# Kernel tuning notes

Measured on AMD Instinct MI355X. Metric: run time of the kernel, lower is better.

The kernel has to match this reference:

```python
import jax, jax.numpy as jnp
import numpy as np

B, N, D = 2, 2048, 1024   # batch, seq, input_dim
H, DK, DV = 8, 128, 1024  # heads, qk_dim, v_dim (v_dim == input_dim for residual)


def setup_inputs() -> dict:
    key = jax.random.key(0)
    kx, kq, kk, kv = jax.random.split(key, 4)
    scale = 0.02
    x = jax.random.normal(kx, (B, N, D), dtype=jnp.float32)
    # torch nn.Linear weights are [out_features, in_features]; stacked over heads.
    Wq = jax.random.normal(kq, (H, DK, D), dtype=jnp.float32) * scale
    Wk = jax.random.normal(kk, (H, DK, D), dtype=jnp.float32) * scale
    Wv = jax.random.normal(kv, (H, DV, D), dtype=jnp.float32) * scale
    return {"x": x, "Wq": Wq, "Wk": Wk, "Wv": Wv}


def reference(x, Wq, Wk, Wv):
    # x: [B, N, D]; Wq/Wk: [H, DK, D]; Wv: [H, DV, D]
    n = x.shape[-2]
    Q = jnp.einsum('bnd,hed->bhne', x, Wq)  # [B,H,N,DK]
    K = jnp.einsum('bnd,hed->bhne', x, Wk)  # [B,H,N,DK]
    V = jnp.einsum('bnd,hvd->bhnv', x, Wv)  # [B,H,N,DV]
    scores = jnp.einsum('bhne,bhme->bhnm', Q, K)  # [B,H,N,N]
    # causal mask: masked entries set to mask_value=0.0, then relu, then /N
    causal = jnp.tril(jnp.ones((n, n), dtype=bool))
    sim = jnp.where(causal, jax.nn.relu(scores), jnp.float32(0.0)) / jnp.float32(n)
    # sum of per-head outputs added to residual
    head_out = jnp.einsum('bhnm,bhmv->bnv', sim, V)  # [B,N,DV]
    return x + head_out
```

## Files before the change

### kernel.cpp

```cpp
#include <hip/hip_runtime.h>

typedef __attribute__((ext_vector_type(8))) short bf16x8;
typedef __attribute__((ext_vector_type(4))) float floatx4;

__device__ __forceinline__ unsigned short f2bf(float f) {
  unsigned int u = __builtin_bit_cast(unsigned int, f);
  unsigned int r = (u + 0x7fffu + ((u >> 16) & 1u)) >> 16;
  return (unsigned short)r;
}

__device__ __forceinline__ unsigned int pack2(float a, float b) {
  return (unsigned int)f2bf(a) | ((unsigned int)f2bf(b) << 16);
}

__device__ __forceinline__ void gload16(const void* g, void* l) {
  __builtin_amdgcn_global_load_lds(
      (__attribute__((address_space(1))) void*)g,
      (__attribute__((address_space(3))) void*)l, 16, 0, 0);
}

__device__ __forceinline__ void barrier_v0_lgkm() {
  asm volatile("s_waitcnt vmcnt(0) lgkmcnt(0)" ::: "memory");
  __builtin_amdgcn_s_barrier();
  __builtin_amdgcn_sched_barrier(0);
}

__global__ __launch_bounds__(256) void convert_all(
    const float4* __restrict__ x4,
    const float4* __restrict__ wq4, const float4* __restrict__ wk4,
    const float4* __restrict__ wv4,
    uint2* __restrict__ xb4, uint2* __restrict__ wqkb4, uint2* __restrict__ wvb4,
    float4* __restrict__ out4)
{
  const int NX = 2 * 2048 * 1024 / 4;
  const int NQK = 8 * 256 * 1024 / 4;
  const int NV = 8 * 1024 * 1024 / 4;
  const int total = NX + NQK + NV;
  const float inv_n = 1.0f / 2048.0f;
  for (int i = blockIdx.x * 256 + threadIdx.x; i < total; i += gridDim.x * 256) {
    float4 f; uint2* dst;
    if (i < NX) {
      f = x4[i]; dst = &xb4[i];
      out4[i] = f;
    } else if (i < NX + NQK) {
      int j = i - NX;
      int c = j & 255;
      int row = j >> 8;
      int h = row >> 8, r = row & 255;
      f = (r < 128) ? wq4[(h * 128 + r) * 256 + c] : wk4[(h * 128 + r - 128) * 256 + c];
      dst = &wqkb4[j];
    } else {
      int j = i - NX - NQK;
      f = wv4[j];
      f.x *= inv_n; f.y *= inv_n; f.z *= inv_n; f.w *= inv_n;
      dst = &wvb4[j];
    }
    uint2 p; p.x = pack2(f.x, f.y); p.y = pack2(f.z, f.w);
    *dst = p;
  }
}

__global__ __launch_bounds__(256) void init_out(const float4* __restrict__ x,
                                                float4* __restrict__ out, int n4) {
  for (int i = blockIdx.x * 256 + threadIdx.x; i < n4; i += gridDim.x * 256)
    out[i] = x[i];
}

__global__ __launch_bounds__(512, 2) void gemm8(
    const unsigned short* __restrict__ xb,
    const unsigned short* __restrict__ Wqkb,
    const unsigned short* __restrict__ Wvb,
    unsigned short* __restrict__ Qb, unsigned short* __restrict__ Kb,
    unsigned short* __restrict__ Vtb)
{
  __shared__ __align__(16) unsigned short LA[2][2][128 * 64];
  __shared__ __align__(16) unsigned short LB[2][2][128 * 64];
  const int bid = blockIdx.x;
  const int t = threadIdx.x;
  const int l = t & 63, w = t >> 6;
  const int l16 = l & 15, lq = l >> 4;
  const int wm = w & 1, wn = w >> 1;

  const unsigned short *Ag, *Bg;
  unsigned short *C0, *C1; long ld0, ld1; int split;
  if (bid < 128) {
    int z = bid & 15, br = bid >> 4;
    int b = z >> 3, h = z & 7;
    Ag = xb + (long)b * 2048 * 1024 + (long)br * 256 * 1024;
    Bg = Wqkb + (long)h * 256 * 1024;
    C0 = Qb + (long)z * 2048 * 128 + (long)br * 256 * 128;
    C1 = Kb + (long)z * 2048 * 128 + (long)br * 256 * 128;
    ld0 = 128; ld1 = 128; split = 128;
  } else {
    int v = bid - 128;
    int z = v & 15, rc = v >> 4;
    int bx = rc & 3, by = rc >> 2;
    int b = z >> 3, h = z & 7;
    Ag = Wvb + (long)h * 1024 * 1024 + (long)bx * 256 * 1024;
    Bg = xb + (long)b * 2048 * 1024 + (long)by * 256 * 1024;
    C0 = Vtb + (long)z * 1024 * 2048 + (long)bx * 256 * 2048 + by * 256;
    C1 = C0; ld0 = 2048; ld1 = 2048; split = 1 << 30;
  }

  int rr[2], kk[2], cb[2];
#pragma unroll
  for (int i = 0; i < 2; i++) {
    int c = i * 512 + t;
    rr[i] = c >> 3;
    int k8 = c & 7;
    kk[i] = (k8 ^ (((rr[i] >> 2) & 3) << 1)) * 8;
    cb[i] = (i * 512 + w * 64) * 8;
  }
  auto STAGE = [&](const unsigned short* OP, unsigned short* dstbuf, int kt, int half) {
#pragma unroll
    for (int i = 0; i < 2; i++)
      gload16(OP + (long)(half * 128 + rr[i]) * 1024 + kt * 64 + kk[i],
              dstbuf + cb[i]);
  };
  auto RD = [&](const unsigned short* buf, int fr, int ks) -> bf16x8 {
    int r = fr * 16 + l16;
    int k8 = ks * 4 + lq;
    int k8s = k8 ^ (((r >> 2) & 3) << 1);
    return *reinterpret_cast<const bf16x8*>(buf + r * 64 + k8s * 8);
  };

  floatx4 acc[8][4] = {};
  const int bfr = (wn & 1) * 4;

  STAGE(Ag, LA[0][0], 0, 0); STAGE(Ag, LA[0][1], 0, 1);
  STAGE(Bg, LB[0][0], 0, 0); STAGE(Bg, LB[0][1], 0, 1);
  asm volatile("s_waitcnt vmcnt(0)" ::: "memory");
  __builtin_amdgcn_s_barrier();
  __builtin_amdgcn_sched_barrier(0);

  for (int kt = 0; kt < 16; kt++) {
    const int d = kt & 1, nd = d ^ 1;
    const unsigned short* myA = LA[d][wm];
    const unsigned short* myB = LB[d][wn >> 1];
    const bool more = (kt + 1 < 16);
    bf16x8 a0[4][2], a1[4][2], b0[2][2], b1[2][2];

#pragma unroll
    for (int fr = 0; fr < 4; fr++)
#pragma unroll
      for (int ks = 0; ks < 2; ks++) a0[fr][ks] = RD(myA, fr, ks);
#pragma unroll
    for (int fc = 0; fc < 2; fc++)
#pragma unroll
      for (int ks = 0; ks < 2; ks++) b0[fc][ks] = RD(myB, bfr + fc, ks);
    if (more) { STAGE(Ag, LA[nd][0], kt + 1, 0); STAGE(Ag, LA[nd][1], kt + 1, 1); }
    __builtin_amdgcn_s_barrier();
    asm volatile("s_waitcnt lgkmcnt(0)" ::: "memory");
    __builtin_amdgcn_sched_barrier(0);
    __builtin_amdgcn_s_setprio(1);
#pragma unroll
    for (int fr = 0; fr < 4; fr++)
#pragma unroll
      for (int fc = 0; fc < 2; fc++)
#pragma unroll
        for (int ks = 0; ks < 2; ks++)
          acc[fr][fc] = __builtin_amdgcn_mfma_f32_16x16x32_bf16(
              a0[fr][ks], b0[fc][ks], acc[fr][fc], 0, 0, 0);
    __builtin_amdgcn_s_setprio(0);
    __builtin_amdgcn_s_barrier();

#pragma unroll
    for (int fc = 0; fc < 2; fc++)
#pragma unroll
      for (int ks = 0; ks < 2; ks++) b1[fc][ks] = RD(myB, bfr + 2 + fc, ks);
    if (more) { STAGE(Bg, LB[nd][0], kt + 1, 0); STAGE(Bg, LB[nd][1], kt + 1, 1); }
    __builtin_amdgcn_s_barrier();
    asm volatile("s_waitcnt lgkmcnt(0)" ::: "memory");
    __builtin_amdgcn_sched_barrier(0);
    __builtin_amdgcn_s_setprio(1);
#pragma unroll
    for (int fr = 0; fr < 4; fr++)
#pragma unroll
      for (int fc = 0; fc < 2; fc++)
#pragma unroll
        for (int ks = 0; ks < 2; ks++)
          acc[fr][2 + fc] = __builtin_amdgcn_mfma_f32_16x16x32_bf16(
              a0[fr][ks], b1[fc][ks], acc[fr][2 + fc], 0, 0, 0);
    __builtin_amdgcn_s_setprio(0);
    __builtin_amdgcn_s_barrier();

#pragma unroll
    for (int fr = 0; fr < 4; fr++)
#pragma unroll
      for (int ks = 0; ks < 2; ks++) a1[fr][ks] = RD(myA, 4 + fr, ks);
    __builtin_amdgcn_s_barrier();
    asm volatile("s_waitcnt lgkmcnt(0)" ::: "memory");
    __builtin_amdgcn_sched_barrier(0);
    __builtin_amdgcn_s_setprio(1);
#pragma unroll
    for (int fr = 0; fr < 4; fr++)
#pragma unroll
      for (int fc = 0; fc < 2; fc++)
#pragma unroll
        for (int ks = 0; ks < 2; ks++)
          acc[4 + fr][fc] = __builtin_amdgcn_mfma_f32_16x16x32_bf16(
              a1[fr][ks], b0[fc][ks], acc[4 + fr][fc], 0, 0, 0);
    __builtin_amdgcn_s_setprio(0);
    __builtin_amdgcn_s_barrier();

    __builtin_amdgcn_s_setprio(1);
#pragma unroll
    for (int fr = 0; fr < 4; fr++)
#pragma unroll
      for (int fc = 0; fc < 2; fc++)
#pragma unroll
        for (int ks = 0; ks < 2; ks++)
          acc[4 + fr][2 + fc] = __builtin_amdgcn_mfma_f32_16x16x32_bf16(
              a1[fr][ks], b1[fc][ks], acc[4 + fr][2 + fc], 0, 0, 0);
    __builtin_amdgcn_s_setprio(0);
    asm volatile("s_waitcnt vmcnt(0)" ::: "memory");
    __builtin_amdgcn_s_barrier();
    __builtin_amdgcn_sched_barrier(0);
  }

#pragma unroll
  for (int fr = 0; fr < 8; fr++)
#pragma unroll
    for (int fc = 0; fc < 4; fc++)
#pragma unroll
      for (int j = 0; j < 4; j++) {
        int row = wm * 128 + fr * 16 + lq * 4 + j;
        int col = wn * 64 + fc * 16 + l16;
        unsigned short v = f2bf(acc[fr][fc][j]);
        if (col < split) C0[(long)row * ld0 + col] = v;
        else             C1[(long)row * ld1 + (col - split)] = v;
      }
}

__global__ __launch_bounds__(256) void gemm_bt(
    const float* __restrict__ Abase, long sAb, long sAh,
    const float* __restrict__ Bbase, long sBb, long sBh,
    unsigned short* __restrict__ Cbase, long sC,
    int M, int Nc, int K, int H, float cscale)
{
  int z = blockIdx.z;
  int b = z / H, h = z % H;
  const float* A  = Abase + (long)b * sAb + (long)h * sAh;
  const float* Bm = Bbase + (long)b * sBb + (long)h * sBh;
  unsigned short* C = Cbase + (long)z * sC;
  int tRow = blockIdx.x * 128;
  int tCol = blockIdx.y * 128;
  __shared__ __align__(16) unsigned short LA[128 * 72];
  __shared__ __align__(16) unsigned short LB[128 * 72];
  int t = threadIdx.x;
  int l = t & 63, w = t >> 6;
  int wr = w >> 1, wc = w & 1;
  int l16 = l & 15, lq = l >> 4;
  floatx4 acc[4][4] = {};
  for (int k0 = 0; k0 < K; k0 += 64) {
    __syncthreads();
    for (int i = 0; i < 8; i++) {
      int lin = i * 256 + t;
      int row = lin >> 4;
      int c4  = lin & 15;
      float4 va = *reinterpret_cast<const float4*>(A + (long)(tRow + row) * K + k0 + c4 * 4);
      uint2 pa; pa.x = pack2(va.x, va.y); pa.y = pack2(va.z, va.w);
      *reinterpret_cast<uint2*>(&LA[row * 72 + c4 * 4]) = pa;
      float4 vb = *reinterpret_cast<const float4*>(Bm + (long)(tCol + row) * K + k0 + c4 * 4);
      uint2 pb; pb.x = pack2(vb.x, vb.y); pb.y = pack2(vb.z, vb.w);
      *reinterpret_cast<uint2*>(&LB[row * 72 + c4 * 4]) = pb;
    }
    __syncthreads();
    for (int kk = 0; kk < 2; kk++) {
      bf16x8 af[4], bfr[4];
      for (int m = 0; m < 4; m++)
        af[m]  = *reinterpret_cast<const bf16x8*>(&LA[(wr * 64 + m * 16 + l16) * 72 + kk * 32 + lq * 8]);
      for (int n = 0; n < 4; n++)
        bfr[n] = *reinterpret_cast<const bf16x8*>(&LB[(wc * 64 + n * 16 + l16) * 72 + kk * 32 + lq * 8]);
      for (int m = 0; m < 4; m++)
        for (int n = 0; n < 4; n++)
          acc[m][n] = __builtin_amdgcn_mfma_f32_16x16x32_bf16(af[m], bfr[n], acc[m][n], 0, 0, 0);
    }
  }
  for (int m = 0; m < 4; m++)
    for (int n = 0; n < 4; n++)
      for (int j = 0; j < 4; j++) {
        int row = tRow + wr * 64 + m * 16 + lq * 4 + j;
        int col = tCol + wc * 64 + n * 16 + l16;
        C[(long)row * Nc + col] = f2bf(acc[m][n][j] * cscale);
      }
}

__global__ __launch_bounds__(256) void gemm_qk(
    const float* __restrict__ x,
    const float* __restrict__ Wq, const float* __restrict__ Wk,
    unsigned short* __restrict__ Qb, unsigned short* __restrict__ Kb)
{
  int z = blockIdx.z;
  int b = z >> 3, h = z & 7;
  const float* A  = x + (long)b * 2048 * 1024;
  const float* Bm = (blockIdx.y ? Wk : Wq) + (long)h * 128 * 1024;
  unsigned short* C = (blockIdx.y ? Kb : Qb) + (long)z * 2048 * 128;
  int tRow = blockIdx.x * 128;
  __shared__ __align__(16) unsigned short LA[128 * 72];
  __shared__ __align__(16) unsigned short LB[128 * 72];
  int t = threadIdx.x;
  int l = t & 63, w = t >> 6;
  int wr = w >> 1, wc = w & 1;
  int l16 = l & 15, lq = l >> 4;
  floatx4 acc[4][4] = {};
  const int K = 1024;
  for (int k0 = 0; k0 < K; k0 += 64) {
    __syncthreads();
    for (int i = 0; i < 8; i++) {
      int lin = i * 256 + t;
      int row = lin >> 4;
      int c4  = lin & 15;
      float4 va = *reinterpret_cast<const float4*>(A + (long)(tRow + row) * K + k0 + c4 * 4);
      uint2 pa; pa.x = pack2(va.x, va.y); pa.y = pack2(va.z, va.w);
      *reinterpret_cast<uint2*>(&LA[row * 72 + c4 * 4]) = pa;
      float4 vb = *reinterpret_cast<const float4*>(Bm + (long)row * K + k0 + c4 * 4);
      uint2 pb; pb.x = pack2(vb.x, vb.y); pb.y = pack2(vb.z, vb.w);
      *reinterpret_cast<uint2*>(&LB[row * 72 + c4 * 4]) = pb;
    }
    __syncthreads();
    for (int kk = 0; kk < 2; kk++) {
      bf16x8 af[4], bfr[4];
      for (int m = 0; m < 4; m++)
        af[m]  = *reinterpret_cast<const bf16x8*>(&LA[(wr * 64 + m * 16 + l16) * 72 + kk * 32 + lq * 8]);
      for (int n = 0; n < 4; n++)
        bfr[n] = *reinterpret_cast<const bf16x8*>(&LB[(wc * 64 + n * 16 + l16) * 72 + kk * 32 + lq * 8]);
      for (int m = 0; m < 4; m++)
        for (int n = 0; n < 4; n++)
          acc[m][n] = __builtin_amdgcn_mfma_f32_16x16x32_bf16(af[m], bfr[n], acc[m][n], 0, 0, 0);
    }
  }
  for (int m = 0; m < 4; m++)
    for (int n = 0; n < 4; n++)
      for (int j = 0; j < 4; j++) {
        int row = tRow + wr * 64 + m * 16 + lq * 4 + j;
        int col = wc * 64 + n * 16 + l16;
        C[(long)row * 128 + col] = f2bf(acc[m][n][j]);
      }
}

__global__ __launch_bounds__(256, 2) void attn_fused(
    const unsigned short* __restrict__ Qb,
    const unsigned short* __restrict__ Kb,
    const unsigned short* __restrict__ Vtb,
    float* __restrict__ out)
{
  const int bid = blockIdx.x;
  const int z = bid & 15;
  const int pair = (bid >> 4) & 15;
  const int vb = bid >> 8;
  const int b = z >> 3;
  const int t = threadIdx.x;
  const int l = t & 63, w = t >> 6;
  const int l16 = l & 15, lq = l >> 4;
  const int wm = w & 1, wn = w >> 1;
  const int swz = l16 & 7;

  __shared__ __align__(16) unsigned short LK[2][64 * 128];
  __shared__ __align__(16) unsigned short LV[256 * 64];
  __shared__ __align__(16) unsigned short LP[64 * 64];

  const unsigned short* Qz = Qb + (long)z * 2048 * 128;
  const unsigned short* Kh = Kb + (long)z * 2048 * 128;
  const unsigned short* Vh = Vtb + (long)z * 1024 * 2048 + (long)(vb * 256) * 2048;

  int ksrc[4], kdst[4];
#pragma unroll
  for (int i = 0; i < 4; i++) {
    int chunk = i * 256 + w * 64 + l;
    int r = chunk >> 4, c = chunk & 15;
    int cs = ((c & 7) ^ (r & 7)) | (c & 8);
    ksrc[i] = r * 128 + cs * 8;
    kdst[i] = (i * 256 + w * 64) * 8;
  }
  int vsrc[8], vdst[8];
#pragma unroll
  for (int i = 0; i < 8; i++) {
    int chunk = i * 256 + w * 64 + l;
    int r = chunk >> 3, c = chunk & 7;
    int cs = c ^ (r & 7);
    vsrc[i] = r * 2048 + cs * 8;
    vdst[i] = (i * 256 + w * 64) * 8;
  }

  int cur = 0;
  for (int hf = 0; hf < 2; hf++) {
    const int T = hf ? (31 - pair) : pair;
    const unsigned short* Qh = Qz + (long)T * 64 * 128;
    bf16x8 aQ[2][4];
#pragma unroll
    for (int sn = 0; sn < 2; sn++)
#pragma unroll
      for (int ke = 0; ke < 4; ke++)
        aQ[sn][ke] = *reinterpret_cast<const bf16x8*>(
            Qh + (long)(wn * 32 + sn * 16 + l16) * 128 + ke * 32 + lq * 8);
    floatx4 acc[4][4] = {};
#pragma unroll
    for (int i = 0; i < 4; i++)
      gload16(Kh + ksrc[i], &LK[cur][kdst[i]]);
    for (int M = 0; M <= T; M++) {
      barrier_v0_lgkm();
#pragma unroll
      for (int i = 0; i < 8; i++)
        gload16(Vh + M * 64 + vsrc[i], &LV[vdst[i]]);
      if (M < T) {
#pragma unroll
        for (int i = 0; i < 4; i++)
          gload16(Kh + (M + 1) * 8192 + ksrc[i], &LK[cur ^ 1][kdst[i]]);
      }
      const unsigned short* LKc = LK[cur];
      floatx4 sacc[2][2] = {{{}, {}}, {{}, {}}};
      __builtin_amdgcn_s_setprio(1);
#pragma unroll
      for (int ke = 0; ke < 4; ke++) {
        bf16x8 kf[2];
#pragma unroll
        for (int sm = 0; sm < 2; sm++) {
          int chunk = 4 * ke + lq;
          kf[sm] = *reinterpret_cast<const bf16x8*>(
              &LKc[(wm * 32 + sm * 16 + l16) * 128 +
                   ((((chunk & 7) ^ swz) | (chunk & 8)) * 8)]);
        }
#pragma unroll
        for (int sm = 0; sm < 2; sm++)
#pragma unroll
          for (int sn = 0; sn < 2; sn++)
            sacc[sm][sn] = __builtin_amdgcn_mfma_f32_16x16x32_bf16(
                kf[sm], aQ[sn][ke], sacc[sm][sn], 0, 0, 0);
      }
      __builtin_amdgcn_s_setprio(0);
      const bool diag = (M == T);
#pragma unroll
      for (int sm = 0; sm < 2; sm++)
#pragma unroll
        for (int sn = 0; sn < 2; sn++) {
          floatx4 v = sacc[sm][sn];
          float f0 = fmaxf(v[0], 0.0f), f1 = fmaxf(v[1], 0.0f);
          float f2 = fmaxf(v[2], 0.0f), f3 = fmaxf(v[3], 0.0f);
          if (diag) {
            int mm = wm * 32 + sm * 16 + lq * 4;
            int nn = wn * 32 + sn * 16 + l16;
            if (mm + 0 > nn) f0 = 0.0f;
            if (mm + 1 > nn) f1 = 0.0f;
            if (mm + 2 > nn) f2 = 0.0f;
            if (mm + 3 > nn) f3 = 0.0f;
          }
          unsigned int p0, p1;
          asm("v_cvt_pk_bf16_f32 %0, %1, %2" : "=v"(p0) : "v"(f0), "v"(f1));
          asm("v_cvt_pk_bf16_f32 %0, %1, %2" : "=v"(p1) : "v"(f2), "v"(f3));
          uint2 pk; pk.x = p0; pk.y = p1;
          int row = wn * 32 + sn * 16 + l16;
          int cs = wm * 32 + sm * 16 + lq * 4;
          *reinterpret_cast<uint2*>(
              &LP[row * 64 + (((cs >> 3) ^ (row & 7)) * 8) + (cs & 7)]) = pk;
        }
      if (M < T) {
        asm volatile("s_waitcnt vmcnt(4) lgkmcnt(0)" ::: "memory");
      } else {
        asm volatile("s_waitcnt vmcnt(0) lgkmcnt(0)" ::: "memory");
      }
      __builtin_amdgcn_s_barrier();
      __builtin_amdgcn_sched_barrier(0);
      __builtin_amdgcn_s_setprio(1);
#pragma unroll
      for (int km = 0; km < 2; km++) {
        bf16x8 aP[4], bV[4];
#pragma unroll
        for (int nf = 0; nf < 4; nf++)
          aP[nf] = *reinterpret_cast<const bf16x8*>(
              &LP[(nf * 16 + l16) * 64 + (((4 * km + lq) ^ swz) * 8)]);
#pragma unroll
        for (int vf = 0; vf < 4; vf++)
          bV[vf] = *reinterpret_cast<const bf16x8*>(
              &LV[(w * 64 + vf * 16 + l16) * 64 + (((4 * km + lq) ^ swz) * 8)]);
#pragma unroll
        for (int nf = 0; nf < 4; nf++)
#pragma unroll
          for (int vf = 0; vf < 4; vf++)
            acc[nf][vf] = __builtin_amdgcn_mfma_f32_16x16x32_bf16(
                aP[nf], bV[vf], acc[nf][vf], 0, 0, 0);
      }
      __builtin_amdgcn_s_setprio(0);
      cur ^= 1;
    }
#pragma unroll
    for (int nf = 0; nf < 4; nf++)
#pragma unroll
      for (int vf = 0; vf < 4; vf++)
#pragma unroll
        for (int j = 0; j < 4; j++) {
          int n = T * 64 + nf * 16 + lq * 4 + j;
          int v = vb * 256 + w * 64 + vf * 16 + l16;
          long idx = ((long)b * 2048 + n) * 1024 + v;
          unsafeAtomicAdd(&out[idx], acc[nf][vf][j]);
        }
  }
}

extern "C" void kernel_launch(void* const* d_in, const int* in_sizes, int n_in,
                              void* d_out, int out_size, void* d_ws, size_t ws_size,
                              hipStream_t stream) {
  const float* x  = (const float*)d_in[0];
  const float* Wq = (const float*)d_in[1];
  const float* Wk = (const float*)d_in[2];
  const float* Wv = (const float*)d_in[3];
  float* out = (float*)d_out;
  const size_t MB = 1u << 20;
  dim3 blk(256);

  if (ws_size >= 104 * MB) {
    unsigned short* Vtb  = (unsigned short*)d_ws;
    unsigned short* Wqkb = (unsigned short*)d_ws;
    unsigned short* Qb   = (unsigned short*)((char*)d_ws + 64 * MB);
    unsigned short* Kb   = (unsigned short*)((char*)d_ws + 72 * MB);
    unsigned short* xb   = (unsigned short*)((char*)d_ws + 80 * MB);
    unsigned short* Wvb  = (unsigned short*)((char*)d_ws + 88 * MB);

    convert_all<<<dim3(2048), blk, 0, stream>>>(
        (const float4*)x, (const float4*)Wq, (const float4*)Wk, (const float4*)Wv,
        (uint2*)xb, (uint2*)Wqkb, (uint2*)Wvb, (float4*)out);
    gemm8<<<dim3(640), dim3(512), 0, stream>>>(xb, Wqkb, Wvb, Qb, Kb, Vtb);
    attn_fused<<<dim3(1024), blk, 0, stream>>>(Qb, Kb, Vtb, out);
  } else {
    unsigned short* Qb  = (unsigned short*)d_ws;
    unsigned short* Kb  = Qb + (size_t)2 * 8 * 2048 * 128;
    unsigned short* Vtb = Kb + (size_t)2 * 8 * 2048 * 128;
    init_out<<<dim3(1024), blk, 0, stream>>>(
        (const float4*)x, (float4*)out, 2 * 2048 * 1024 / 4);
    gemm_qk<<<dim3(16, 2, 16), blk, 0, stream>>>(x, Wq, Wk, Qb, Kb);
    gemm_bt<<<dim3(8, 16, 16), blk, 0, stream>>>(
        Wv, 0, (long)1024 * 1024, x, (long)2048 * 1024, 0,
        Vtb, (long)1024 * 2048, 1024, 2048, 1024, 8, 1.0f / 2048.0f);
    attn_fused<<<dim3(1024), blk, 0, stream>>>(Qb, Kb, Vtb, out);
  }
}
```

Baseline: 277.5 us.

## Double attention query tile to 128 rows to halve K/V reloads

The fused attention kernel now processes 128 query rows per block instead of 64, with each wave covering 64 query columns. Every K and V tile loaded into shared memory is reused across twice as many queries, which halves K/V global traffic and the number of atomic-add passes over the output. The grid shrinks from 1024 to 512 blocks. The costs are higher accumulator register pressure (8x4 fragments), a larger shared P buffer, and extra masked work on the two diagonal tiles, all of which may reduce occupancy.

```diff
diff --git a/kernel.cpp b/kernel.cpp
--- a/kernel.cpp
+++ b/kernel.cpp
@@ -347,8 +347,8 @@
 {
   const int bid = blockIdx.x;
   const int z = bid & 15;
-  const int pair = (bid >> 4) & 15;
-  const int vb = bid >> 8;
+  const int qp = (bid >> 4) & 7;
+  const int vb = bid >> 7;
   const int b = z >> 3;
   const int t = threadIdx.x;
   const int l = t & 63, w = t >> 6;
@@ -358,7 +358,7 @@
 
   __shared__ __align__(16) unsigned short LK[2][64 * 128];
   __shared__ __align__(16) unsigned short LV[256 * 64];
-  __shared__ __align__(16) unsigned short LP[64 * 64];
+  __shared__ __align__(16) unsigned short LP[128 * 64];
 
   const unsigned short* Qz = Qb + (long)z * 2048 * 128;
   const unsigned short* Kh = Kb + (long)z * 2048 * 128;
@@ -385,31 +385,32 @@
 
   int cur = 0;
   for (int hf = 0; hf < 2; hf++) {
-    const int T = hf ? (31 - pair) : pair;
-    const unsigned short* Qh = Qz + (long)T * 64 * 128;
-    bf16x8 aQ[2][4];
-#pragma unroll
-    for (int sn = 0; sn < 2; sn++)
+    const int qb = hf ? (15 - qp) : qp;
+    const int MT = 2 * qb + 1;
+    const unsigned short* Qh = Qz + (long)qb * 128 * 128;
+    bf16x8 aQ[4][4];
+#pragma unroll
+    for (int sn = 0; sn < 4; sn++)
 #pragma unroll
       for (int ke = 0; ke < 4; ke++)
         aQ[sn][ke] = *reinterpret_cast<const bf16x8*>(
-            Qh + (long)(wn * 32 + sn * 16 + l16) * 128 + ke * 32 + lq * 8);
-    floatx4 acc[4][4] = {};
+            Qh + (long)(wn * 64 + sn * 16 + l16) * 128 + ke * 32 + lq * 8);
+    floatx4 acc[8][4] = {};
 #pragma unroll
     for (int i = 0; i < 4; i++)
       gload16(Kh + ksrc[i], &LK[cur][kdst[i]]);
-    for (int M = 0; M <= T; M++) {
+    for (int M = 0; M <= MT; M++) {
       barrier_v0_lgkm();
 #pragma unroll
       for (int i = 0; i < 8; i++)
         gload16(Vh + M * 64 + vsrc[i], &LV[vdst[i]]);
-      if (M < T) {
+      if (M < MT) {
 #pragma unroll
         for (int i = 0; i < 4; i++)
           gload16(Kh + (M + 1) * 8192 + ksrc[i], &LK[cur ^ 1][kdst[i]]);
       }
       const unsigned short* LKc = LK[cur];
-      floatx4 sacc[2][2] = {{{}, {}}, {{}, {}}};
+      floatx4 sacc[2][4] = {};
       __builtin_amdgcn_s_setprio(1);
 #pragma unroll
       for (int ke = 0; ke < 4; ke++) {
@@ -424,22 +425,23 @@
 #pragma unroll
         for (int sm = 0; sm < 2; sm++)
 #pragma unroll
-          for (int sn = 0; sn < 2; sn++)
+          for (int sn = 0; sn < 4; sn++)
             sacc[sm][sn] = __builtin_amdgcn_mfma_f32_16x16x32_bf16(
                 kf[sm], aQ[sn][ke], sacc[sm][sn], 0, 0, 0);
       }
       __builtin_amdgcn_s_setprio(0);
-      const bool diag = (M == T);
+      const bool diag = (M >= 2 * qb);
+      const int mbase = (M - 2 * qb) * 64;
 #pragma unroll
       for (int sm = 0; sm < 2; sm++)
 #pragma unroll
-        for (int sn = 0; sn < 2; sn++) {
+        for (int sn = 0; sn < 4; sn++) {
           floatx4 v = sacc[sm][sn];
           float f0 = fmaxf(v[0], 0.0f), f1 = fmaxf(v[1], 0.0f);
           float f2 = fmaxf(v[2], 0.0f), f3 = fmaxf(v[3], 0.0f);
           if (diag) {
-            int mm = wm * 32 + sm * 16 + lq * 4;
-            int nn = wn * 32 + sn * 16 + l16;
+            int mm = mbase + wm * 32 + sm * 16 + lq * 4;
+            int nn = wn * 64 + sn * 16 + l16;
             if (mm + 0 > nn) f0 = 0.0f;
             if (mm + 1 > nn) f1 = 0.0f;
             if (mm + 2 > nn) f2 = 0.0f;
@@ -449,12 +451,12 @@
           asm("v_cvt_pk_bf16_f32 %0, %1, %2" : "=v"(p0) : "v"(f0), "v"(f1));
           asm("v_cvt_pk_bf16_f32 %0, %1, %2" : "=v"(p1) : "v"(f2), "v"(f3));
           uint2 pk; pk.x = p0; pk.y = p1;
-          int row = wn * 32 + sn * 16 + l16;
+          int row = wn * 64 + sn * 16 + l16;
           int cs = wm * 32 + sm * 16 + lq * 4;
           *reinterpret_cast<uint2*>(
               &LP[row * 64 + (((cs >> 3) ^ (row & 7)) * 8) + (cs & 7)]) = pk;
         }
-      if (M < T) {
+      if (M < MT) {
         asm volatile("s_waitcnt vmcnt(4) lgkmcnt(0)" ::: "memory");
       } else {
         asm volatile("s_waitcnt vmcnt(0) lgkmcnt(0)" ::: "memory");
@@ -464,32 +466,32 @@
       __builtin_amdgcn_s_setprio(1);
 #pragma unroll
       for (int km = 0; km < 2; km++) {
-        bf16x8 aP[4], bV[4];
-#pragma unroll
-        for (int nf = 0; nf < 4; nf++)
-          aP[nf] = *reinterpret_cast<const bf16x8*>(
-              &LP[(nf * 16 + l16) * 64 + (((4 * km + lq) ^ swz) * 8)]);
+        bf16x8 bV[4];
 #pragma unroll
         for (int vf = 0; vf < 4; vf++)
           bV[vf] = *reinterpret_cast<const bf16x8*>(
               &LV[(w * 64 + vf * 16 + l16) * 64 + (((4 * km + lq) ^ swz) * 8)]);
 #pragma unroll
-        for (int nf = 0; nf < 4; nf++)
+        for (int nf = 0; nf < 8; nf++) {
+          int row = nf * 16 + l16;
+          bf16x8 aP = *reinterpret_cast<const bf16x8*>(
+              &LP[row * 64 + (((4 * km + lq) ^ (row & 7)) * 8)]);
 #pragma unroll
           for (int vf = 0; vf < 4; vf++)
             acc[nf][vf] = __builtin_amdgcn_mfma_f32_16x16x32_bf16(
-                aP[nf], bV[vf], acc[nf][vf], 0, 0, 0);
+                aP, bV[vf], acc[nf][vf], 0, 0, 0);
+        }
       }
       __builtin_amdgcn_s_setprio(0);
       cur ^= 1;
     }
 #pragma unroll
-    for (int nf = 0; nf < 4; nf++)
+    for (int nf = 0; nf < 8; nf++)
 #pragma unroll
       for (int vf = 0; vf < 4; vf++)
 #pragma unroll
         for (int j = 0; j < 4; j++) {
-          int n = T * 64 + nf * 16 + lq * 4 + j;
+          int n = qb * 128 + nf * 16 + lq * 4 + j;
           int v = vb * 256 + w * 64 + vf * 16 + l16;
           long idx = ((long)b * 2048 + n) * 1024 + v;
           unsafeAtomicAdd(&out[idx], acc[nf][vf][j]);
@@ -520,7 +522,7 @@
         (const float4*)x, (const float4*)Wq, (const float4*)Wk, (const float4*)Wv,
         (uint2*)xb, (uint2*)Wqkb, (uint2*)Wvb, (float4*)out);
     gemm8<<<dim3(640), dim3(512), 0, stream>>>(xb, Wqkb, Wvb, Qb, Kb, Vtb);
-    attn_fused<<<dim3(1024), blk, 0, stream>>>(Qb, Kb, Vtb, out);
+    attn_fused<<<dim3(512), blk, 0, stream>>>(Qb, Kb, Vtb, out);
   } else {
     unsigned short* Qb  = (unsigned short*)d_ws;
     unsigned short* Kb  = Qb + (size_t)2 * 8 * 2048 * 128;
@@ -531,6 +533,6 @@
     gemm_bt<<<dim3(8, 16, 16), blk, 0, stream>>>(
         Wv, 0, (long)1024 * 1024, x, (long)2048 * 1024, 0,
         Vtb, (long)1024 * 2048, 1024, 2048, 1024, 8, 1.0f / 2048.0f);
-    attn_fused<<<dim3(1024), blk, 0, stream>>>(Qb, Kb, Vtb, out);
-  }
-}
+    attn_fused<<<dim3(512), blk, 0, stream>>>(Qb, Kb, Vtb, out);
+  }
+}
```

New measurement: 425.5 us. +53.3%, slower.

## Widen attention key tile to 128 with 512-thread blocks

Applied to the files above, without the earlier changes.

The fused attention kernel now uses 8 waves per block and processes 128 keys per iteration instead of 64. This halves the number of loop iterations, barriers and pipeline steps per query tile. Each wave now owns 32 value columns instead of 64, and the score computation is split across 4 key-row groups. The cost is larger LDS buffers, about 144KB per block, so only one block fits per CU. The final 128-key chunk of even-indexed query tiles is half wasted on fully masked work.

```diff
diff --git a/kernel.cpp b/kernel.cpp
--- a/kernel.cpp
+++ b/kernel.cpp
@@ -339,7 +339,7 @@
       }
 }
 
-__global__ __launch_bounds__(256, 2) void attn_fused(
+__global__ __launch_bounds__(512) void attn_fused(
     const unsigned short* __restrict__ Qb,
     const unsigned short* __restrict__ Kb,
     const unsigned short* __restrict__ Vtb,
@@ -353,12 +353,11 @@
   const int t = threadIdx.x;
   const int l = t & 63, w = t >> 6;
   const int l16 = l & 15, lq = l >> 4;
-  const int wm = w & 1, wn = w >> 1;
-  const int swz = l16 & 7;
-
-  __shared__ __align__(16) unsigned short LK[2][64 * 128];
-  __shared__ __align__(16) unsigned short LV[256 * 64];
-  __shared__ __align__(16) unsigned short LP[64 * 64];
+  const int wm = w & 3, wn = w >> 2;
+
+  __shared__ __align__(16) unsigned short LK[2][128 * 128];
+  __shared__ __align__(16) unsigned short LV[256 * 128];
+  __shared__ __align__(16) unsigned short LP[64 * 128];
 
   const unsigned short* Qz = Qb + (long)z * 2048 * 128;
   const unsigned short* Kh = Kb + (long)z * 2048 * 128;
@@ -367,25 +366,26 @@
   int ksrc[4], kdst[4];
 #pragma unroll
   for (int i = 0; i < 4; i++) {
-    int chunk = i * 256 + w * 64 + l;
+    int chunk = i * 512 + t;
     int r = chunk >> 4, c = chunk & 15;
     int cs = ((c & 7) ^ (r & 7)) | (c & 8);
     ksrc[i] = r * 128 + cs * 8;
-    kdst[i] = (i * 256 + w * 64) * 8;
+    kdst[i] = (i * 512 + w * 64) * 8;
   }
   int vsrc[8], vdst[8];
 #pragma unroll
   for (int i = 0; i < 8; i++) {
-    int chunk = i * 256 + w * 64 + l;
-    int r = chunk >> 3, c = chunk & 7;
-    int cs = c ^ (r & 7);
+    int chunk = i * 512 + t;
+    int r = chunk >> 4, c = chunk & 15;
+    int cs = ((c & 7) ^ (r & 7)) | (c & 8);
     vsrc[i] = r * 2048 + cs * 8;
-    vdst[i] = (i * 256 + w * 64) * 8;
+    vdst[i] = (i * 512 + w * 64) * 8;
   }
 
   int cur = 0;
   for (int hf = 0; hf < 2; hf++) {
     const int T = hf ? (31 - pair) : pair;
+    const int nsteps = (T >> 1) + 1;
     const unsigned short* Qh = Qz + (long)T * 64 * 128;
     bf16x8 aQ[2][4];
 #pragma unroll
@@ -394,19 +394,19 @@
       for (int ke = 0; ke < 4; ke++)
         aQ[sn][ke] = *reinterpret_cast<const bf16x8*>(
             Qh + (long)(wn * 32 + sn * 16 + l16) * 128 + ke * 32 + lq * 8);
-    floatx4 acc[4][4] = {};
+    floatx4 acc[4][2] = {};
 #pragma unroll
     for (int i = 0; i < 4; i++)
       gload16(Kh + ksrc[i], &LK[cur][kdst[i]]);
-    for (int M = 0; M <= T; M++) {
+    for (int M = 0; M < nsteps; M++) {
       barrier_v0_lgkm();
 #pragma unroll
       for (int i = 0; i < 8; i++)
-        gload16(Vh + M * 64 + vsrc[i], &LV[vdst[i]]);
-      if (M < T) {
+        gload16(Vh + M * 128 + vsrc[i], &LV[vdst[i]]);
+      if (M + 1 < nsteps) {
 #pragma unroll
         for (int i = 0; i < 4; i++)
-          gload16(Kh + (M + 1) * 8192 + ksrc[i], &LK[cur ^ 1][kdst[i]]);
+          gload16(Kh + (M + 1) * 16384 + ksrc[i], &LK[cur ^ 1][kdst[i]]);
       }
       const unsigned short* LKc = LK[cur];
       floatx4 sacc[2][2] = {{{}, {}}, {{}, {}}};
@@ -416,10 +416,10 @@
         bf16x8 kf[2];
 #pragma unroll
         for (int sm = 0; sm < 2; sm++) {
-          int chunk = 4 * ke + lq;
-          kf[sm] = *reinterpret_cast<const bf16x8*>(
-              &LKc[(wm * 32 + sm * 16 + l16) * 128 +
-                   ((((chunk & 7) ^ swz) | (chunk & 8)) * 8)]);
+          int row = wm * 32 + sm * 16 + l16;
+          int c = 4 * ke + lq;
+          int chs = ((c & 7) ^ (row & 7)) | (c & 8);
+          kf[sm] = *reinterpret_cast<const bf16x8*>(&LKc[row * 128 + chs * 8]);
         }
 #pragma unroll
         for (int sm = 0; sm < 2; sm++)
@@ -429,7 +429,8 @@
                 kf[sm], aQ[sn][ke], sacc[sm][sn], 0, 0, 0);
       }
       __builtin_amdgcn_s_setprio(0);
-      const bool diag = (M == T);
+      const bool diag = (M == nsteps - 1);
+      const int mmbase = M * 128 - T * 64 + wm * 32;
 #pragma unroll
       for (int sm = 0; sm < 2; sm++)
 #pragma unroll
@@ -438,7 +439,7 @@
           float f0 = fmaxf(v[0], 0.0f), f1 = fmaxf(v[1], 0.0f);
           float f2 = fmaxf(v[2], 0.0f), f3 = fmaxf(v[3], 0.0f);
           if (diag) {
-            int mm = wm * 32 + sm * 16 + lq * 4;
+            int mm = mmbase + sm * 16 + lq * 4;
             int nn = wn * 32 + sn * 16 + l16;
             if (mm + 0 > nn) f0 = 0.0f;
             if (mm + 1 > nn) f1 = 0.0f;
@@ -451,10 +452,11 @@
           uint2 pk; pk.x = p0; pk.y = p1;
           int row = wn * 32 + sn * 16 + l16;
           int cs = wm * 32 + sm * 16 + lq * 4;
-          *reinterpret_cast<uint2*>(
-              &LP[row * 64 + (((cs >> 3) ^ (row & 7)) * 8) + (cs & 7)]) = pk;
+          int ch = cs >> 3;
+          int chs = ((ch & 7) ^ (row & 7)) | (ch & 8);
+          *reinterpret_cast<uint2*>(&LP[row * 128 + chs * 8 + (cs & 7)]) = pk;
         }
-      if (M < T) {
+      if (M + 1 < nsteps) {
         asm volatile("s_waitcnt vmcnt(4) lgkmcnt(0)" ::: "memory");
       } else {
         asm volatile("s_waitcnt vmcnt(0) lgkmcnt(0)" ::: "memory");
@@ -463,20 +465,26 @@
       __builtin_amdgcn_sched_barrier(0);
       __builtin_amdgcn_s_setprio(1);
 #pragma unroll
-      for (int km = 0; km < 2; km++) {
-        bf16x8 aP[4], bV[4];
+      for (int km = 0; km < 4; km++) {
+        bf16x8 aP[4], bV[2];
+#pragma unroll
+        for (int nf = 0; nf < 4; nf++) {
+          int row = nf * 16 + l16;
+          int c = 4 * km + lq;
+          int chs = ((c & 7) ^ (row & 7)) | (c & 8);
+          aP[nf] = *reinterpret_cast<const bf16x8*>(&LP[row * 128 + chs * 8]);
+        }
+#pragma unroll
+        for (int vf = 0; vf < 2; vf++) {
+          int row = w * 32 + vf * 16 + l16;
+          int c = 4 * km + lq;
+          int chs = ((c & 7) ^ (row & 7)) | (c & 8);
+          bV[vf] = *reinterpret_cast<const bf16x8*>(&LV[row * 128 + chs * 8]);
+        }
 #pragma unroll
         for (int nf = 0; nf < 4; nf++)
-          aP[nf] = *reinterpret_cast<const bf16x8*>(
-              &LP[(nf * 16 + l16) * 64 + (((4 * km + lq) ^ swz) * 8)]);
-#pragma unroll
-        for (int vf = 0; vf < 4; vf++)
-          bV[vf] = *reinterpret_cast<const bf16x8*>(
-              &LV[(w * 64 + vf * 16 + l16) * 64 + (((4 * km + lq) ^ swz) * 8)]);
-#pragma unroll
-        for (int nf = 0; nf < 4; nf++)
-#pragma unroll
-          for (int vf = 0; vf < 4; vf++)
+#pragma unroll
+          for (int vf = 0; vf < 2; vf++)
             acc[nf][vf] = __builtin_amdgcn_mfma_f32_16x16x32_bf16(
                 aP[nf], bV[vf], acc[nf][vf], 0, 0, 0);
       }
@@ -486,11 +494,11 @@
 #pragma unroll
     for (int nf = 0; nf < 4; nf++)
 #pragma unroll
-      for (int vf = 0; vf < 4; vf++)
+      for (int vf = 0; vf < 2; vf++)
 #pragma unroll
         for (int j = 0; j < 4; j++) {
           int n = T * 64 + nf * 16 + lq * 4 + j;
-          int v = vb * 256 + w * 64 + vf * 16 + l16;
+          int v = vb * 256 + w * 32 + vf * 16 + l16;
           long idx = ((long)b * 2048 + n) * 1024 + v;
           unsafeAtomicAdd(&out[idx], acc[nf][vf][j]);
         }
@@ -520,7 +528,7 @@
         (const float4*)x, (const float4*)Wq, (const float4*)Wk, (const float4*)Wv,
         (uint2*)xb, (uint2*)Wqkb, (uint2*)Wvb, (float4*)out);
     gemm8<<<dim3(640), dim3(512), 0, stream>>>(xb, Wqkb, Wvb, Qb, Kb, Vtb);
-    attn_fused<<<dim3(1024), blk, 0, stream>>>(Qb, Kb, Vtb, out);
+    attn_fused<<<dim3(1024), dim3(512), 0, stream>>>(Qb, Kb, Vtb, out);
   } else {
     unsigned short* Qb  = (unsigned short*)d_ws;
     unsigned short* Kb  = Qb + (size_t)2 * 8 * 2048 * 128;
@@ -531,6 +539,6 @@
     gemm_bt<<<dim3(8, 16, 16), blk, 0, stream>>>(
         Wv, 0, (long)1024 * 1024, x, (long)2048 * 1024, 0,
         Vtb, (long)1024 * 2048, 1024, 2048, 1024, 8, 1.0f / 2048.0f);
-    attn_fused<<<dim3(1024), blk, 0, stream>>>(Qb, Kb, Vtb, out);
-  }
-}
+    attn_fused<<<dim3(1024), dim3(512), 0, stream>>>(Qb, Kb, Vtb, out);
+  }
+}
```

Measured after the change: 328.0 us. 18.2% more time.
